# Kernel tuning notes

Hardware: AMD Instinct MI355X
Metric: run time of the kernel (lower is better)

The kernel has to match this reference:

```python
import jax, jax.numpy as jnp
import numpy as np

N = 50000
E = 800000
NEG_SLOPE = 0.2


def setup_inputs() -> dict:
    key = jax.random.key(0)
    ks = jax.random.split(key, 12)
    feat = jax.random.normal(ks[0], (N, 256), dtype=jnp.float32)
    src = jax.random.randint(ks[1], (E,), 0, N, dtype=jnp.int32)
    dst = jax.random.randint(ks[2], (E,), 0, N, dtype=jnp.int32)
    # layer 1: in=256 -> H=4, D=64 (concat 256)
    W1 = jax.random.normal(ks[3], (256, 256), dtype=jnp.float32) * (1.0 / np.sqrt(256))
    attn_l1 = jax.random.normal(ks[4], (4, 64), dtype=jnp.float32) * 0.1
    attn_r1 = jax.random.normal(ks[5], (4, 64), dtype=jnp.float32) * 0.1
    bias1 = jnp.zeros((256,), dtype=jnp.float32)
    # layer 2: in=256 -> H=1, D=128
    W2 = jax.random.normal(ks[6], (256, 128), dtype=jnp.float32) * (1.0 / np.sqrt(256))
    attn_l2 = jax.random.normal(ks[7], (1, 128), dtype=jnp.float32) * 0.1
    attn_r2 = jax.random.normal(ks[8], (1, 128), dtype=jnp.float32) * 0.1
    bias2 = jnp.zeros((128,), dtype=jnp.float32)
    return {"feat": feat, "src": src, "dst": dst,
            "W1": W1, "attn_l1": attn_l1, "attn_r1": attn_r1, "bias1": bias1,
            "W2": W2, "attn_l2": attn_l2, "attn_r2": attn_r2, "bias2": bias2}


def gat_conv(feat, src, dst, W, attn_l, attn_r, bias, apply_relu):
    H, D = attn_l.shape
    n = feat.shape[0]
    ft = (feat @ W).reshape(n, H, D)                      # [N,H,D]
    el = jnp.einsum('nhd,hd->nh', ft, attn_l)             # [N,H]
    er = jnp.einsum('nhd,hd->nh', ft, attn_r)             # [N,H]
    e = el[src] + er[dst]                                 # [E,H]  u_add_v
    e = jnp.where(e > 0, e, NEG_SLOPE * e)                # leaky_relu
    # edge softmax grouped by dst
    m = jax.ops.segment_max(e, dst, num_segments=n)       # [N,H]
    ex = jnp.exp(e - m[dst])
    denom = jax.ops.segment_sum(ex, dst, num_segments=n)  # [N,H]
    a = ex / denom[dst]                                   # [E,H]
    msg = ft[src] * a[:, :, None]                         # [E,H,D]
    out = jax.ops.segment_sum(msg, dst, num_segments=n)   # [N,H,D]
    out = out + bias.reshape(1, H, D)
    out = out.reshape(n, H * D)                           # concat_out
    if apply_relu:
        out = jax.nn.relu(out)
    return out


def reference(feat, src, dst, W1, attn_l1, attn_r1, bias1, W2, attn_l2, attn_r2, bias2):
    h = gat_conv(feat, src, dst, W1, attn_l1, attn_r1, bias1, apply_relu=True)
    h = gat_conv(h, src, dst, W2, attn_l2, attn_r2, bias2, apply_relu=False)
    return h
```

## Files before the change

kernel.cpp:

```cpp
#include <hip/hip_runtime.h>
#include <hip/hip_bf16.h>

#define NEG_SLOPE 0.2f

typedef short s16x8 __attribute__((ext_vector_type(8)));
typedef float f32x4 __attribute__((ext_vector_type(4)));

__device__ __forceinline__ unsigned short f2bf(float f) {
    unsigned int u = __float_as_uint(f);
    unsigned int r = (u + 0x7fffu + ((u >> 16) & 1u)) >> 16;
    return (unsigned short)r;
}
__device__ __forceinline__ float bf2f(unsigned int us) {
    return __uint_as_float(us << 16);
}


__global__ void count_wl_k(const int* __restrict__ dst, int* __restrict__ counts, int E,
                           const float* __restrict__ W1, const float* __restrict__ al1,
                           const float* __restrict__ ar1,
                           const float* __restrict__ W2, const float* __restrict__ al2,
                           const float* __restrict__ ar2,
                           float* __restrict__ wl1, float* __restrict__ wl2) {
    if (blockIdx.x == 0) {
        int k = threadIdx.x;
        #pragma unroll
        for (int h = 0; h < 4; h++) {
            float sl = 0.f, sr = 0.f;
            #pragma unroll 8
            for (int d = 0; d < 64; d++) {
                float wv = W1[k * 256 + h * 64 + d];
                sl = fmaf(wv, al1[h * 64 + d], sl);
                sr = fmaf(wv, ar1[h * 64 + d], sr);
            }
            wl1[k * 8 + h] = sl;
            wl1[k * 8 + 4 + h] = sr;
        }
        float sl = 0.f, sr = 0.f;
        #pragma unroll 8
        for (int d = 0; d < 128; d++) {
            float wv = W2[k * 128 + d];
            sl = fmaf(wv, al2[d], sl);
            sr = fmaf(wv, ar2[d], sr);
        }
        wl2[k * 2 + 0] = sl;
        wl2[k * 2 + 1] = sr;
        return;
    }
    int e = (blockIdx.x - 1) * 256 + threadIdx.x;
    if (e < E) atomicAdd(&counts[dst[e]], 1);
}


__global__ __launch_bounds__(1024) void scan_k(const int* __restrict__ counts,
                                               int* __restrict__ flags,
                                               int* __restrict__ offsets,
                                               int* __restrict__ cursor, int n) {
    __shared__ int s_wt[16];
    __shared__ int s_base;
    const int tid = threadIdx.x, lane = tid & 63, wid = tid >> 6;
    const int bid = blockIdx.x;
    const int i = bid * 1024 + tid;
    int v = (i < n) ? counts[i] : 0;
    int incl = v;
    #pragma unroll
    for (int o = 1; o < 64; o <<= 1) {
        int t = __shfl_up(incl, o);
        if (lane >= o) incl += t;
    }
    if (lane == 63) s_wt[wid] = incl;
    __syncthreads();
    if (tid == 0) {
        int r = 0;
        #pragma unroll
        for (int w = 0; w < 16; w++) { int t = s_wt[w]; s_wt[w] = r; r += t; }
        atomicExch(&flags[bid], r + 1);
        s_base = 0;
    }
    __syncthreads();
    if (wid == 0) {
        int contrib = 0;
        if (lane < bid) {
            int f;
            while ((f = atomicAdd(&flags[lane], 0)) == 0) {}
            contrib = f - 1;
        }
        #pragma unroll
        for (int o = 32; o > 0; o >>= 1) contrib += __shfl_xor(contrib, o);
        if (lane == 0) s_base = contrib;
    }
    __syncthreads();
    if (i < n) {
        int excl = s_base + s_wt[wid] + (incl - v);
        offsets[i + 1] = excl + v;
        cursor[i] = excl;
    }
    if (bid == 0 && tid == 0) offsets[0] = 0;
}

__global__ void fill_csr_k(const int* __restrict__ src, const int* __restrict__ dst,
                           int* __restrict__ cursor, int* __restrict__ csr_src, int E) {
    int e = blockIdx.x * blockDim.x + threadIdx.x;
    if (e < E) {
        int pos = atomicAdd(&cursor[dst[e]], 1);
        csr_src[pos] = src[e];
    }
}


template <int MODE>
__global__ __launch_bounds__(256) void gemm_k(const float* __restrict__ A,
                                              const float* __restrict__ B,
                                              unsigned short* __restrict__ Cb,
                                              int M, int K, int Nc,
                                              const float* __restrict__ wl,
                                              float* __restrict__ el,
                                              float* __restrict__ er) {
    __shared__ __align__(16) unsigned short As_hi[128][40], As_lo[128][40];
    __shared__ __align__(16) unsigned short Bs_hi[64][40],  Bs_lo[64][40];
    __shared__ float s_wla[256], s_wlb[256];
    __shared__ float s_red[128][2];

    const int tid = threadIdx.x;
    const int lane = tid & 63, wid = tid >> 6;
    const int by = blockIdx.x;
    const int row0 = blockIdx.y * 128;
    const int col0 = by * 64;
    const int wm = (wid & 1) * 64;
    const int wn = (wid >> 1) * 32;
    const int quad = lane >> 4, mrow = lane & 15;

    const int a_r = tid >> 1;
    const int a_k = (tid & 1) * 16;
    const int b_k = tid >> 3;
    const int b_n = (tid & 7) * 8;
    const bool a_valid = (row0 + a_r) < M;

    if (MODE == 1) { s_wla[tid] = wl[tid * 8 + by]; s_wlb[tid] = wl[tid * 8 + 4 + by]; }
    else           { s_wla[tid] = wl[tid * 2 + by]; }
    __syncthreads();

    f32x4 acc[4][2];
    #pragma unroll
    for (int i = 0; i < 4; i++)
        #pragma unroll
        for (int j = 0; j < 2; j++) acc[i][j] = f32x4{0.f, 0.f, 0.f, 0.f};
    float pa = 0.f, pb = 0.f;

    for (int k0 = 0; k0 < K; k0 += 32) {
        float af[16];
        if (a_valid) {
            const float* ap = &A[(size_t)(row0 + a_r) * K + k0 + a_k];
            #pragma unroll
            for (int q = 0; q < 4; q++) {
                float4 t = *(const float4*)(ap + q * 4);
                af[q * 4 + 0] = t.x; af[q * 4 + 1] = t.y;
                af[q * 4 + 2] = t.z; af[q * 4 + 3] = t.w;
            }
        } else {
            #pragma unroll
            for (int q = 0; q < 16; q++) af[q] = 0.f;
        }
        #pragma unroll
        for (int p = 0; p < 16; p++) {
            pa = fmaf(af[p], s_wla[k0 + a_k + p], pa);
            if (MODE == 1) pb = fmaf(af[p], s_wlb[k0 + a_k + p], pb);
        }
        unsigned int* dh = (unsigned int*)&As_hi[a_r][a_k];
        unsigned int* dl = (unsigned int*)&As_lo[a_r][a_k];
        #pragma unroll
        for (int p = 0; p < 8; p++) {
            unsigned short h0 = f2bf(af[2 * p]), h1 = f2bf(af[2 * p + 1]);
            unsigned short l0 = f2bf(af[2 * p] - bf2f(h0));
            unsigned short l1 = f2bf(af[2 * p + 1] - bf2f(h1));
            dh[p] = (unsigned int)h0 | ((unsigned int)h1 << 16);
            dl[p] = (unsigned int)l0 | ((unsigned int)l1 << 16);
        }
        {
            const float* bp = &B[(size_t)(k0 + b_k) * Nc + col0 + b_n];
            float4 t0 = *(const float4*)(bp);
            float4 t1 = *(const float4*)(bp + 4);
            float bf[8] = {t0.x, t0.y, t0.z, t0.w, t1.x, t1.y, t1.z, t1.w};
            #pragma unroll
            for (int x = 0; x < 8; x++) {
                unsigned short h = f2bf(bf[x]);
                unsigned short l = f2bf(bf[x] - bf2f(h));
                Bs_hi[b_n + x][b_k] = h;
                Bs_lo[b_n + x][b_k] = l;
            }
        }
        __syncthreads();

        s16x8 ah[4], al4[4], bh[2], bl[2];
        #pragma unroll
        for (int i = 0; i < 4; i++) {
            ah[i]  = *(const s16x8*)&As_hi[wm + 16 * i + mrow][quad * 8];
            al4[i] = *(const s16x8*)&As_lo[wm + 16 * i + mrow][quad * 8];
        }
        #pragma unroll
        for (int j = 0; j < 2; j++) {
            bh[j] = *(const s16x8*)&Bs_hi[wn + 16 * j + mrow][quad * 8];
            bl[j] = *(const s16x8*)&Bs_lo[wn + 16 * j + mrow][quad * 8];
        }
        #pragma unroll
        for (int i = 0; i < 4; i++)
            #pragma unroll
            for (int j = 0; j < 2; j++) {
                acc[i][j] = __builtin_amdgcn_mfma_f32_16x16x32_bf16(ah[i],  bh[j], acc[i][j], 0, 0, 0);
                acc[i][j] = __builtin_amdgcn_mfma_f32_16x16x32_bf16(ah[i],  bl[j], acc[i][j], 0, 0, 0);
                acc[i][j] = __builtin_amdgcn_mfma_f32_16x16x32_bf16(al4[i], bh[j], acc[i][j], 0, 0, 0);
            }
        __syncthreads();
    }

    if (a_k == 16) { s_red[a_r][0] = pa; if (MODE == 1) s_red[a_r][1] = pb; }
    __syncthreads();
    if (a_k == 0 && a_valid) {
        float ra = pa + s_red[a_r][0];
        if (MODE == 1) {
            float rb = pb + s_red[a_r][1];
            el[(row0 + a_r) * 4 + by] = ra;
            er[(row0 + a_r) * 4 + by] = rb;
        } else {
            (by == 0 ? el : er)[row0 + a_r] = ra;
        }
    }

    #pragma unroll
    for (int i = 0; i < 4; i++) {
        #pragma unroll
        for (int j = 0; j < 2; j++) {
            int col = col0 + wn + 16 * j + mrow;
            int rbase = row0 + wm + 16 * i + quad * 4;
            #pragma unroll
            for (int r = 0; r < 4; r++) {
                int row = rbase + r;
                if (row < M) Cb[(size_t)row * Nc + col] = f2bf(acc[i][j][r]);
            }
        }
    }
}


__device__ __forceinline__ void fma8(float* acc, float wgt, uint4 u) {
    acc[0] = fmaf(wgt, bf2f(u.x & 0xffff), acc[0]);
    acc[1] = fmaf(wgt, bf2f(u.x >> 16),    acc[1]);
    acc[2] = fmaf(wgt, bf2f(u.y & 0xffff), acc[2]);
    acc[3] = fmaf(wgt, bf2f(u.y >> 16),    acc[3]);
    acc[4] = fmaf(wgt, bf2f(u.z & 0xffff), acc[4]);
    acc[5] = fmaf(wgt, bf2f(u.z >> 16),    acc[5]);
    acc[6] = fmaf(wgt, bf2f(u.w & 0xffff), acc[6]);
    acc[7] = fmaf(wgt, bf2f(u.w >> 16),    acc[7]);
}

template <int H, int D, bool RELU>
__global__ __launch_bounds__(256) void fagg_k(const unsigned short* __restrict__ ft,
                                              const float* __restrict__ el,
                                              const float* __restrict__ er,
                                              const int* __restrict__ offsets,
                                              const int* __restrict__ csr_src,
                                              const float* __restrict__ bias,
                                              float* __restrict__ out, int n_nodes) {
    constexpr int HD = H * D;
    constexpr int LPE = HD / 8;
    constexpr int EPI = 64 / LPE;
    const int lane = threadIdx.x & 63;
    const int w = threadIdx.x >> 6;
    const int n = blockIdx.x * 4 + w;
    __shared__ int   s_src[4][64];
    __shared__ float s_a[4][64 * H];
    if (n >= n_nodes) return;
    const int off = offsets[n];
    const int deg = offsets[n + 1] - off;
    const int lane_sub = lane & (LPE - 1);
    const int q = lane / LPE;
    const int c0 = lane_sub * 8;
    const int h_of = c0 / D;

    float ern[H];
    #pragma unroll
    for (int h = 0; h < H; h++) ern[h] = er[n * H + h];

    float acc[8];
    #pragma unroll
    for (int t = 0; t < 8; t++) acc[t] = 0.f;

    const int* s_src_w = s_src[w];
    const float* s_a_w = s_a[w];
    const uint4* fp = ((const uint4*)ft) + lane_sub;

    if (deg <= 64) {
        const bool act = lane < deg;
        int sv = act ? csr_src[off + lane] : 0;
        s_src[w][lane] = sv;
        float evr[H];
        if constexpr (H == 4) {
            float4 e4 = ((const float4*)el)[sv];
            evr[0] = e4.x; evr[1] = e4.y; evr[2] = e4.z; evr[3] = e4.w;
        } else {
            evr[0] = el[sv];
        }
        int p0, p1, p2, p3;
        {
            p0 = s_src_w[q]; p1 = s_src_w[EPI + q];
            p2 = s_src_w[2 * EPI + q]; p3 = s_src_w[3 * EPI + q];
        }
        uint4 u0 = fp[(size_t)p0 * LPE];
        uint4 u1 = fp[(size_t)p1 * LPE];
        uint4 u2 = fp[(size_t)p2 * LPE];
        uint4 u3 = fp[(size_t)p3 * LPE];
        float ev[H], m[H];
        #pragma unroll
        for (int h = 0; h < H; h++) {
            float t = evr[h] + ern[h];
            t = t > 0.f ? t : NEG_SLOPE * t;
            ev[h] = act ? t : -1e30f;
            m[h] = ev[h];
        }
        #pragma unroll
        for (int h = 0; h < H; h++)
            for (int o = 32; o > 0; o >>= 1) m[h] = fmaxf(m[h], __shfl_xor(m[h], o));
        float ex[H], sm[H];
        #pragma unroll
        for (int h = 0; h < H; h++) { ex[h] = act ? __expf(ev[h] - m[h]) : 0.f; sm[h] = ex[h]; }
        #pragma unroll
        for (int h = 0; h < H; h++)
            for (int o = 32; o > 0; o >>= 1) sm[h] += __shfl_xor(sm[h], o);
        #pragma unroll
        for (int h = 0; h < H; h++)
            s_a[w][lane * H + h] = ex[h] * (sm[h] > 0.f ? 1.f / sm[h] : 0.f);
        fma8(acc, s_a_w[(q) * H + h_of], u0);
        fma8(acc, s_a_w[(EPI + q) * H + h_of], u1);
        fma8(acc, s_a_w[(2 * EPI + q) * H + h_of], u2);
        fma8(acc, s_a_w[(3 * EPI + q) * H + h_of], u3);
        const int rc = (deg + EPI - 1) & ~(EPI - 1);
        int i = 4 * EPI;
        for (; i + 4 * EPI <= rc; i += 4 * EPI) {
            int e0 = i + q, e1 = i + EPI + q, e2 = i + 2 * EPI + q, e3 = i + 3 * EPI + q;
            int s0 = s_src_w[e0], s1 = s_src_w[e1], s2 = s_src_w[e2], s3 = s_src_w[e3];
            uint4 v0 = fp[(size_t)s0 * LPE];
            uint4 v1 = fp[(size_t)s1 * LPE];
            uint4 v2 = fp[(size_t)s2 * LPE];
            uint4 v3 = fp[(size_t)s3 * LPE];
            float w0 = s_a_w[e0 * H + h_of], w1 = s_a_w[e1 * H + h_of];
            float w2 = s_a_w[e2 * H + h_of], w3 = s_a_w[e3 * H + h_of];
            fma8(acc, w0, v0); fma8(acc, w1, v1); fma8(acc, w2, v2); fma8(acc, w3, v3);
        }
        for (; i < rc; i += EPI) {
            int e = i + q;
            int s = s_src_w[e];
            uint4 v = fp[(size_t)s * LPE];
            fma8(acc, s_a_w[e * H + h_of], v);
        }
    } else {
        float m[H];
        #pragma unroll
        for (int h = 0; h < H; h++) m[h] = -1e30f;
        for (int i = lane; i < deg; i += 64) {
            int sv = csr_src[off + i];
            if constexpr (H == 4) {
                float4 e4 = ((const float4*)el)[sv];
                float tmp[4] = {e4.x, e4.y, e4.z, e4.w};
                #pragma unroll
                for (int h = 0; h < 4; h++) {
                    float t = tmp[h] + ern[h];
                    t = t > 0.f ? t : NEG_SLOPE * t;
                    m[h] = fmaxf(m[h], t);
                }
            } else {
                float t = el[sv] + ern[0];
                t = t > 0.f ? t : NEG_SLOPE * t;
                m[0] = fmaxf(m[0], t);
            }
        }
        #pragma unroll
        for (int h = 0; h < H; h++)
            for (int o = 32; o > 0; o >>= 1) m[h] = fmaxf(m[h], __shfl_xor(m[h], o));
        float sm[H];
        #pragma unroll
        for (int h = 0; h < H; h++) sm[h] = 0.f;
        for (int i = lane; i < deg; i += 64) {
            int sv = csr_src[off + i];
            if constexpr (H == 4) {
                float4 e4 = ((const float4*)el)[sv];
                float tmp[4] = {e4.x, e4.y, e4.z, e4.w};
                #pragma unroll
                for (int h = 0; h < 4; h++) {
                    float t = tmp[h] + ern[h];
                    t = t > 0.f ? t : NEG_SLOPE * t;
                    sm[h] += __expf(t - m[h]);
                }
            } else {
                float t = el[sv] + ern[0];
                t = t > 0.f ? t : NEG_SLOPE * t;
                sm[0] += __expf(t - m[0]);
            }
        }
        #pragma unroll
        for (int h = 0; h < H; h++)
            for (int o = 32; o > 0; o >>= 1) sm[h] += __shfl_xor(sm[h], o);
        float inv[H];
        #pragma unroll
        for (int h = 0; h < H; h++) inv[h] = (sm[h] > 0.f) ? (1.f / sm[h]) : 0.f;
        for (int base = 0; base < deg; base += 64) {
            const bool act2 = base + lane < deg;
            int sv = act2 ? csr_src[off + base + lane] : 0;
            s_src[w][lane] = sv;
            float exh[H];
            if constexpr (H == 4) {
                float4 e4 = ((const float4*)el)[sv];
                float tmp[4] = {e4.x, e4.y, e4.z, e4.w};
                #pragma unroll
                for (int h = 0; h < 4; h++) {
                    float t = tmp[h] + ern[h];
                    t = t > 0.f ? t : NEG_SLOPE * t;
                    exh[h] = act2 ? __expf(t - m[h]) * inv[h] : 0.f;
                }
            } else {
                float t = el[sv] + ern[0];
                t = t > 0.f ? t : NEG_SLOPE * t;
                exh[0] = act2 ? __expf(t - m[0]) * inv[0] : 0.f;
            }
            #pragma unroll
            for (int h = 0; h < H; h++) s_a[w][lane * H + h] = exh[h];
            int cnt = min(64, deg - base);
            int rc = (cnt + EPI - 1) & ~(EPI - 1);
            int i = 0;
            for (; i + 4 * EPI <= rc; i += 4 * EPI) {
                int e0 = i + q, e1 = i + EPI + q, e2 = i + 2 * EPI + q, e3 = i + 3 * EPI + q;
                int s0 = s_src_w[e0], s1 = s_src_w[e1], s2 = s_src_w[e2], s3 = s_src_w[e3];
                uint4 v0 = fp[(size_t)s0 * LPE];
                uint4 v1 = fp[(size_t)s1 * LPE];
                uint4 v2 = fp[(size_t)s2 * LPE];
                uint4 v3 = fp[(size_t)s3 * LPE];
                float w0 = s_a_w[e0 * H + h_of], w1 = s_a_w[e1 * H + h_of];
                float w2 = s_a_w[e2 * H + h_of], w3 = s_a_w[e3 * H + h_of];
                fma8(acc, w0, v0); fma8(acc, w1, v1); fma8(acc, w2, v2); fma8(acc, w3, v3);
            }
            for (; i < rc; i += EPI) {
                int e = i + q;
                int s = s_src_w[e];
                uint4 v = fp[(size_t)s * LPE];
                fma8(acc, s_a_w[e * H + h_of], v);
            }
        }
    }

    #pragma unroll
    for (int t = 0; t < 8; t++) {
        #pragma unroll
        for (int s = LPE; s < 64; s <<= 1) acc[t] += __shfl_xor(acc[t], s);
    }
    if (lane < LPE) {
        float4 b0 = ((const float4*)bias)[lane * 2];
        float4 b1 = ((const float4*)bias)[lane * 2 + 1];
        float4 o0{acc[0] + b0.x, acc[1] + b0.y, acc[2] + b0.z, acc[3] + b0.w};
        float4 o1{acc[4] + b1.x, acc[5] + b1.y, acc[6] + b1.z, acc[7] + b1.w};
        if (RELU) {
            o0.x = fmaxf(o0.x, 0.f); o0.y = fmaxf(o0.y, 0.f);
            o0.z = fmaxf(o0.z, 0.f); o0.w = fmaxf(o0.w, 0.f);
            o1.x = fmaxf(o1.x, 0.f); o1.y = fmaxf(o1.y, 0.f);
            o1.z = fmaxf(o1.z, 0.f); o1.w = fmaxf(o1.w, 0.f);
        }
        float4* op = (float4*)out + (size_t)n * (HD / 4) + lane * 2;
        op[0] = o0;
        op[1] = o1;
    }
}


extern "C" void kernel_launch(void* const* d_in, const int* in_sizes, int n_in,
                              void* d_out, int out_size, void* d_ws, size_t ws_size,
                              hipStream_t stream) {
    const float* feat    = (const float*)d_in[0];
    const int*   src     = (const int*)d_in[1];
    const int*   dst     = (const int*)d_in[2];
    const float* W1      = (const float*)d_in[3];
    const float* attn_l1 = (const float*)d_in[4];
    const float* attn_r1 = (const float*)d_in[5];
    const float* bias1   = (const float*)d_in[6];
    const float* W2      = (const float*)d_in[7];
    const float* attn_l2 = (const float*)d_in[8];
    const float* attn_r2 = (const float*)d_in[9];
    const float* bias2   = (const float*)d_in[10];
    float* out = (float*)d_out;

    const int N = in_sizes[0] / 256;
    const int E = in_sizes[1];
    const int NB = (N + 1023) / 1024;

    char* ws = (char*)d_ws;
    size_t o = 0;
    auto alloc = [&](size_t bytes) -> void* {
        void* p = ws + o;
        o = (o + bytes + 255) & ~(size_t)255;
        return p;
    };
    int* counts  = (int*)alloc((size_t)(N + 64) * 4);
    int* flags   = counts + N;
    int* cursor  = (int*)alloc((size_t)N * 4);
    int* offsets = (int*)alloc((size_t)(N + 1) * 4);
    int* csr_src = (int*)alloc((size_t)E * 4);
    float* wl1 = (float*)alloc(256 * 8 * 4);
    float* wl2 = (float*)alloc(256 * 2 * 4);
    float* el1 = (float*)alloc((size_t)N * 4 * 4);
    float* er1 = (float*)alloc((size_t)N * 4 * 4);
    float* el2 = (float*)alloc((size_t)N * 4);
    float* er2 = (float*)alloc((size_t)N * 4);
    unsigned short* ft1b = (unsigned short*)alloc((size_t)N * 256 * 2);
    float* h1 = (float*)alloc((size_t)N * 256 * 4);
    unsigned short* ft2b = ft1b;

    hipMemsetAsync(counts, 0, (size_t)(N + 64) * 4, stream);
    count_wl_k<<<1 + (E + 255) / 256, 256, 0, stream>>>(dst, counts, E,
        W1, attn_l1, attn_r1, W2, attn_l2, attn_r2, wl1, wl2);
    scan_k<<<NB, 1024, 0, stream>>>(counts, flags, offsets, cursor, N);
    fill_csr_k<<<(E + 255) / 256, 256, 0, stream>>>(src, dst, cursor, csr_src, E);

    gemm_k<1><<<dim3(4, (N + 127) / 128), 256, 0, stream>>>(feat, W1, ft1b, N, 256, 256,
                                                            wl1, el1, er1);
    fagg_k<4, 64, true><<<(N + 3) / 4, 256, 0, stream>>>(ft1b, el1, er1, offsets, csr_src,
                                                         bias1, h1, N);

    gemm_k<2><<<dim3(2, (N + 127) / 128), 256, 0, stream>>>(h1, W2, ft2b, N, 256, 128,
                                                            wl2, el2, er2);
    fagg_k<1, 128, false><<<(N + 3) / 4, 256, 0, stream>>>(ft2b, el2, er2, offsets, csr_src,
                                                           bias2, out, N);
}
```

Before: 381.5 us.

## Pre-split operands to bf16 hi/lo and fuse layer-2 prep into aggregation epilogue

```diff
diff --git a/kernel.cpp b/kernel.cpp
--- a/kernel.cpp
+++ b/kernel.cpp
@@ -1,5 +1,4 @@
 #include <hip/hip_runtime.h>
-#include <hip/hip_bf16.h>
 
 #define NEG_SLOPE 0.2f
 
@@ -21,8 +20,11 @@
                            const float* __restrict__ ar1,
                            const float* __restrict__ W2, const float* __restrict__ al2,
                            const float* __restrict__ ar2,
-                           float* __restrict__ wl1, float* __restrict__ wl2) {
-    if (blockIdx.x == 0) {
+                           float* __restrict__ wl1, float* __restrict__ wl2,
+                           unsigned short* __restrict__ Bt1h, unsigned short* __restrict__ Bt1l,
+                           unsigned short* __restrict__ Bt2h, unsigned short* __restrict__ Bt2l) {
+    const int b = blockIdx.x;
+    if (b == 0) {
         int k = threadIdx.x;
         #pragma unroll
         for (int h = 0; h < 4; h++) {
@@ -47,7 +49,35 @@
         wl2[k * 2 + 1] = sr;
         return;
     }
-    int e = (blockIdx.x - 1) * 256 + threadIdx.x;
+    if (b <= 4) {
+        int c = (b - 1) * 64 + (threadIdx.x >> 2);
+        int kq = threadIdx.x & 3;
+        #pragma unroll 8
+        for (int kk = 0; kk < 64; kk++) {
+            int k = kq + kk * 4;
+            float w = W1[k * 256 + c];
+            unsigned short h = f2bf(w);
+            unsigned short l = f2bf(w - bf2f(h));
+            Bt1h[c * 256 + k] = h;
+            Bt1l[c * 256 + k] = l;
+        }
+        return;
+    }
+    if (b <= 6) {
+        int c = (b - 5) * 64 + (threadIdx.x >> 2);
+        int kq = threadIdx.x & 3;
+        #pragma unroll 8
+        for (int kk = 0; kk < 64; kk++) {
+            int k = kq + kk * 4;
+            float w = W2[k * 128 + c];
+            unsigned short h = f2bf(w);
+            unsigned short l = f2bf(w - bf2f(h));
+            Bt2h[c * 256 + k] = h;
+            Bt2l[c * 256 + k] = l;
+        }
+        return;
+    }
+    int e = (b - 7) * 256 + threadIdx.x;
     if (e < E) atomicAdd(&counts[dst[e]], 1);
 }
 
@@ -108,99 +138,121 @@
 }
 
 
-template <int MODE>
-__global__ __launch_bounds__(256) void gemm_k(const float* __restrict__ A,
-                                              const float* __restrict__ B,
+__global__ __launch_bounds__(256) void prep_k(const float* __restrict__ feat,
+                                              const float* __restrict__ wl1,
+                                              unsigned short* __restrict__ Ah,
+                                              unsigned short* __restrict__ Al,
+                                              float* __restrict__ el1,
+                                              float* __restrict__ er1, int Nn) {
+    const int lane = threadIdx.x & 63, wid = threadIdx.x >> 6;
+    const int n = blockIdx.x * 4 + wid;
+    if (n >= Nn) return;
+    float4 f = ((const float4*)(feat + (size_t)n * 256))[lane];
+    unsigned short h0 = f2bf(f.x), h1 = f2bf(f.y), h2 = f2bf(f.z), h3 = f2bf(f.w);
+    unsigned short l0 = f2bf(f.x - bf2f(h0)), l1 = f2bf(f.y - bf2f(h1));
+    unsigned short l2 = f2bf(f.z - bf2f(h2)), l3 = f2bf(f.w - bf2f(h3));
+    uint2 hv, lv;
+    hv.x = (unsigned)h0 | ((unsigned)h1 << 16);
+    hv.y = (unsigned)h2 | ((unsigned)h3 << 16);
+    lv.x = (unsigned)l0 | ((unsigned)l1 << 16);
+    lv.y = (unsigned)l2 | ((unsigned)l3 << 16);
+    ((uint2*)(Ah + (size_t)n * 256))[lane] = hv;
+    ((uint2*)(Al + (size_t)n * 256))[lane] = lv;
+
+    float ff[4] = {f.x, f.y, f.z, f.w};
+    float pa[4] = {0.f, 0.f, 0.f, 0.f}, pb[4] = {0.f, 0.f, 0.f, 0.f};
+    const float* wp = wl1 + lane * 32;
+    #pragma unroll
+    for (int j = 0; j < 4; j++) {
+        float4 wa = *(const float4*)(wp + j * 8);
+        float4 wb = *(const float4*)(wp + j * 8 + 4);
+        pa[0] = fmaf(ff[j], wa.x, pa[0]); pa[1] = fmaf(ff[j], wa.y, pa[1]);
+        pa[2] = fmaf(ff[j], wa.z, pa[2]); pa[3] = fmaf(ff[j], wa.w, pa[3]);
+        pb[0] = fmaf(ff[j], wb.x, pb[0]); pb[1] = fmaf(ff[j], wb.y, pb[1]);
+        pb[2] = fmaf(ff[j], wb.z, pb[2]); pb[3] = fmaf(ff[j], wb.w, pb[3]);
+    }
+    #pragma unroll
+    for (int h = 0; h < 4; h++) {
+        #pragma unroll
+        for (int o = 32; o > 0; o >>= 1) {
+            pa[h] += __shfl_xor(pa[h], o);
+            pb[h] += __shfl_xor(pb[h], o);
+        }
+    }
+    if (lane == 0) {
+        ((float4*)el1)[n] = float4{pa[0], pa[1], pa[2], pa[3]};
+        ((float4*)er1)[n] = float4{pb[0], pb[1], pb[2], pb[3]};
+    }
+}
+
+
+__global__ __launch_bounds__(256) void gemm_k(const unsigned short* __restrict__ Ah,
+                                              const unsigned short* __restrict__ Al,
+                                              const unsigned short* __restrict__ Bh,
+                                              const unsigned short* __restrict__ Bl,
                                               unsigned short* __restrict__ Cb,
-                                              int M, int K, int Nc,
-                                              const float* __restrict__ wl,
-                                              float* __restrict__ el,
-                                              float* __restrict__ er) {
-    __shared__ __align__(16) unsigned short As_hi[128][40], As_lo[128][40];
-    __shared__ __align__(16) unsigned short Bs_hi[64][40],  Bs_lo[64][40];
-    __shared__ float s_wla[256], s_wlb[256];
-    __shared__ float s_red[128][2];
+                                              int M, int Nc) {
+    __shared__ __align__(16) unsigned short As_h[128][56], As_l[128][56];
+    __shared__ __align__(16) unsigned short Bs_h[64][56], Bs_l[64][56];
 
     const int tid = threadIdx.x;
     const int lane = tid & 63, wid = tid >> 6;
-    const int by = blockIdx.x;
     const int row0 = blockIdx.y * 128;
-    const int col0 = by * 64;
+    const int col0 = blockIdx.x * 64;
     const int wm = (wid & 1) * 64;
     const int wn = (wid >> 1) * 32;
     const int quad = lane >> 4, mrow = lane & 15;
 
-    const int a_r = tid >> 1;
+    const int a_row = tid >> 1;
     const int a_k = (tid & 1) * 16;
-    const int b_k = tid >> 3;
-    const int b_n = (tid & 7) * 8;
-    const bool a_valid = (row0 + a_r) < M;
-
-    if (MODE == 1) { s_wla[tid] = wl[tid * 8 + by]; s_wlb[tid] = wl[tid * 8 + 4 + by]; }
-    else           { s_wla[tid] = wl[tid * 2 + by]; }
-    __syncthreads();
+    const int b_col = tid >> 2;
+    const int b_k = (tid & 3) * 8;
+
+    const size_t a_off = (size_t)min(row0 + a_row, M - 1) * 256 + a_k;
+    const size_t b_off = (size_t)(col0 + b_col) * 256 + b_k;
 
     f32x4 acc[4][2];
     #pragma unroll
     for (int i = 0; i < 4; i++)
         #pragma unroll
         for (int j = 0; j < 2; j++) acc[i][j] = f32x4{0.f, 0.f, 0.f, 0.f};
-    float pa = 0.f, pb = 0.f;
-
-    for (int k0 = 0; k0 < K; k0 += 32) {
-        float af[16];
-        if (a_valid) {
-            const float* ap = &A[(size_t)(row0 + a_r) * K + k0 + a_k];
-            #pragma unroll
-            for (int q = 0; q < 4; q++) {
-                float4 t = *(const float4*)(ap + q * 4);
-                af[q * 4 + 0] = t.x; af[q * 4 + 1] = t.y;
-                af[q * 4 + 2] = t.z; af[q * 4 + 3] = t.w;
-            }
-        } else {
-            #pragma unroll
-            for (int q = 0; q < 16; q++) af[q] = 0.f;
-        }
-        #pragma unroll
-        for (int p = 0; p < 16; p++) {
-            pa = fmaf(af[p], s_wla[k0 + a_k + p], pa);
-            if (MODE == 1) pb = fmaf(af[p], s_wlb[k0 + a_k + p], pb);
-        }
-        unsigned int* dh = (unsigned int*)&As_hi[a_r][a_k];
-        unsigned int* dl = (unsigned int*)&As_lo[a_r][a_k];
-        #pragma unroll
-        for (int p = 0; p < 8; p++) {
-            unsigned short h0 = f2bf(af[2 * p]), h1 = f2bf(af[2 * p + 1]);
-            unsigned short l0 = f2bf(af[2 * p] - bf2f(h0));
-            unsigned short l1 = f2bf(af[2 * p + 1] - bf2f(h1));
-            dh[p] = (unsigned int)h0 | ((unsigned int)h1 << 16);
-            dl[p] = (unsigned int)l0 | ((unsigned int)l1 << 16);
-        }
-        {
-            const float* bp = &B[(size_t)(k0 + b_k) * Nc + col0 + b_n];
-            float4 t0 = *(const float4*)(bp);
-            float4 t1 = *(const float4*)(bp + 4);
-            float bf[8] = {t0.x, t0.y, t0.z, t0.w, t1.x, t1.y, t1.z, t1.w};
-            #pragma unroll
-            for (int x = 0; x < 8; x++) {
-                unsigned short h = f2bf(bf[x]);
-                unsigned short l = f2bf(bf[x] - bf2f(h));
-                Bs_hi[b_n + x][b_k] = h;
-                Bs_lo[b_n + x][b_k] = l;
-            }
-        }
+
+    uint4 rah0 = *(const uint4*)(Ah + a_off);
+    uint4 rah1 = *(const uint4*)(Ah + a_off + 8);
+    uint4 ral0 = *(const uint4*)(Al + a_off);
+    uint4 ral1 = *(const uint4*)(Al + a_off + 8);
+    uint4 rbh  = *(const uint4*)(Bh + b_off);
+    uint4 rbl  = *(const uint4*)(Bl + b_off);
+
+    for (int kt = 0; kt < 8; kt++) {
         __syncthreads();
-
+        *(uint4*)&As_h[a_row][a_k]     = rah0;
+        *(uint4*)&As_h[a_row][a_k + 8] = rah1;
+        *(uint4*)&As_l[a_row][a_k]     = ral0;
+        *(uint4*)&As_l[a_row][a_k + 8] = ral1;
+        *(uint4*)&Bs_h[b_col][b_k] = rbh;
+        *(uint4*)&Bs_l[b_col][b_k] = rbl;
+        __syncthreads();
+        if (kt < 7) {
+            size_t ao = a_off + (size_t)(kt + 1) * 32;
+            size_t bo = b_off + (size_t)(kt + 1) * 32;
+            rah0 = *(const uint4*)(Ah + ao);
+            rah1 = *(const uint4*)(Ah + ao + 8);
+            ral0 = *(const uint4*)(Al + ao);
+            ral1 = *(const uint4*)(Al + ao + 8);
+            rbh  = *(const uint4*)(Bh + bo);
+            rbl  = *(const uint4*)(Bl + bo);
+        }
         s16x8 ah[4], al4[4], bh[2], bl[2];
         #pragma unroll
         for (int i = 0; i < 4; i++) {
-            ah[i]  = *(const s16x8*)&As_hi[wm + 16 * i + mrow][quad * 8];
-            al4[i] = *(const s16x8*)&As_lo[wm + 16 * i + mrow][quad * 8];
+            ah[i]  = *(const s16x8*)&As_h[wm + 16 * i + mrow][quad * 8];
+            al4[i] = *(const s16x8*)&As_l[wm + 16 * i + mrow][quad * 8];
         }
         #pragma unroll
         for (int j = 0; j < 2; j++) {
-            bh[j] = *(const s16x8*)&Bs_hi[wn + 16 * j + mrow][quad * 8];
-            bl[j] = *(const s16x8*)&Bs_lo[wn + 16 * j + mrow][quad * 8];
+            bh[j] = *(const s16x8*)&Bs_h[wn + 16 * j + mrow][quad * 8];
+            bl[j] = *(const s16x8*)&Bs_l[wn + 16 * j + mrow][quad * 8];
         }
         #pragma unroll
         for (int i = 0; i < 4; i++)
@@ -210,20 +262,6 @@
                 acc[i][j] = __builtin_amdgcn_mfma_f32_16x16x32_bf16(ah[i],  bl[j], acc[i][j], 0, 0, 0);
                 acc[i][j] = __builtin_amdgcn_mfma_f32_16x16x32_bf16(al4[i], bh[j], acc[i][j], 0, 0, 0);
             }
-        __syncthreads();
-    }
-
-    if (a_k == 16) { s_red[a_r][0] = pa; if (MODE == 1) s_red[a_r][1] = pb; }
-    __syncthreads();
-    if (a_k == 0 && a_valid) {
-        float ra = pa + s_red[a_r][0];
-        if (MODE == 1) {
-            float rb = pb + s_red[a_r][1];
-            el[(row0 + a_r) * 4 + by] = ra;
-            er[(row0 + a_r) * 4 + by] = rb;
-        } else {
-            (by == 0 ? el : er)[row0 + a_r] = ra;
-        }
     }
 
     #pragma unroll
@@ -253,14 +291,19 @@
     acc[7] = fmaf(wgt, bf2f(u.w >> 16),    acc[7]);
 }
 
-template <int H, int D, bool RELU>
+template <int H, int D, bool RELU, bool FUSE2>
 __global__ __launch_bounds__(256) void fagg_k(const unsigned short* __restrict__ ft,
                                               const float* __restrict__ el,
                                               const float* __restrict__ er,
                                               const int* __restrict__ offsets,
                                               const int* __restrict__ csr_src,
                                               const float* __restrict__ bias,
-                                              float* __restrict__ out, int n_nodes) {
+                                              float* __restrict__ out, int n_nodes,
+                                              unsigned short* __restrict__ oh,
+                                              unsigned short* __restrict__ ol,
+                                              const float* __restrict__ wl2,
+                                              float* __restrict__ el2,
+                                              float* __restrict__ er2) {
     constexpr int HD = H * D;
     constexpr int LPE = HD / 8;
     constexpr int EPI = 64 / LPE;
@@ -454,17 +497,50 @@
     if (lane < LPE) {
         float4 b0 = ((const float4*)bias)[lane * 2];
         float4 b1 = ((const float4*)bias)[lane * 2 + 1];
-        float4 o0{acc[0] + b0.x, acc[1] + b0.y, acc[2] + b0.z, acc[3] + b0.w};
-        float4 o1{acc[4] + b1.x, acc[5] + b1.y, acc[6] + b1.z, acc[7] + b1.w};
+        float v[8] = {acc[0] + b0.x, acc[1] + b0.y, acc[2] + b0.z, acc[3] + b0.w,
+                      acc[4] + b1.x, acc[5] + b1.y, acc[6] + b1.z, acc[7] + b1.w};
         if (RELU) {
-            o0.x = fmaxf(o0.x, 0.f); o0.y = fmaxf(o0.y, 0.f);
-            o0.z = fmaxf(o0.z, 0.f); o0.w = fmaxf(o0.w, 0.f);
-            o1.x = fmaxf(o1.x, 0.f); o1.y = fmaxf(o1.y, 0.f);
-            o1.z = fmaxf(o1.z, 0.f); o1.w = fmaxf(o1.w, 0.f);
-        }
-        float4* op = (float4*)out + (size_t)n * (HD / 4) + lane * 2;
-        op[0] = o0;
-        op[1] = o1;
+            #pragma unroll
+            for (int t = 0; t < 8; t++) v[t] = fmaxf(v[t], 0.f);
+        }
+        if constexpr (FUSE2) {
+            unsigned short hh[8], ll[8];
+            #pragma unroll
+            for (int t = 0; t < 8; t++) {
+                hh[t] = f2bf(v[t]);
+                ll[t] = f2bf(v[t] - bf2f(hh[t]));
+            }
+            uint4 hv, lv;
+            hv.x = (unsigned)hh[0] | ((unsigned)hh[1] << 16);
+            hv.y = (unsigned)hh[2] | ((unsigned)hh[3] << 16);
+            hv.z = (unsigned)hh[4] | ((unsigned)hh[5] << 16);
+            hv.w = (unsigned)hh[6] | ((unsigned)hh[7] << 16);
+            lv.x = (unsigned)ll[0] | ((unsigned)ll[1] << 16);
+            lv.y = (unsigned)ll[2] | ((unsigned)ll[3] << 16);
+            lv.z = (unsigned)ll[4] | ((unsigned)ll[5] << 16);
+            lv.w = (unsigned)ll[6] | ((unsigned)ll[7] << 16);
+            ((uint4*)(oh + (size_t)n * HD))[lane] = hv;
+            ((uint4*)(ol + (size_t)n * HD))[lane] = lv;
+            float pa = 0.f, pb = 0.f;
+            #pragma unroll
+            for (int t = 0; t < 8; t++) {
+                float2 wv = ((const float2*)wl2)[lane * 8 + t];
+                pa = fmaf(v[t], wv.x, pa);
+                pb = fmaf(v[t], wv.y, pb);
+            }
+            #pragma unroll
+            for (int o = 16; o > 0; o >>= 1) {
+                pa += __shfl_xor(pa, o);
+                pb += __shfl_xor(pb, o);
+            }
+            if (lane == 0) { el2[n] = pa; er2[n] = pb; }
+        } else {
+            float4 o0{v[0], v[1], v[2], v[3]};
+            float4 o1{v[4], v[5], v[6], v[7]};
+            float4* op = (float4*)out + (size_t)n * (HD / 4) + lane * 2;
+            op[0] = o0;
+            op[1] = o1;
+        }
     }
 }
 
@@ -508,22 +584,31 @@
     float* el2 = (float*)alloc((size_t)N * 4);
     float* er2 = (float*)alloc((size_t)N * 4);
     unsigned short* ft1b = (unsigned short*)alloc((size_t)N * 256 * 2);
-    float* h1 = (float*)alloc((size_t)N * 256 * 4);
+    unsigned short* Ah   = (unsigned short*)alloc((size_t)N * 256 * 2);
+    unsigned short* Al   = (unsigned short*)alloc((size_t)N * 256 * 2);
+    unsigned short* Bt1h = (unsigned short*)alloc((size_t)256 * 256 * 2);
+    unsigned short* Bt1l = (unsigned short*)alloc((size_t)256 * 256 * 2);
+    unsigned short* Bt2h = (unsigned short*)alloc((size_t)128 * 256 * 2);
+    unsigned short* Bt2l = (unsigned short*)alloc((size_t)128 * 256 * 2);
     unsigned short* ft2b = ft1b;
+    unsigned short* h1h  = Ah;
+    unsigned short* h1l  = Al;
 
     hipMemsetAsync(counts, 0, (size_t)(N + 64) * 4, stream);
-    count_wl_k<<<1 + (E + 255) / 256, 256, 0, stream>>>(dst, counts, E,
-        W1, attn_l1, attn_r1, W2, attn_l2, attn_r2, wl1, wl2);
+    count_wl_k<<<7 + (E + 255) / 256, 256, 0, stream>>>(dst, counts, E,
+        W1, attn_l1, attn_r1, W2, attn_l2, attn_r2, wl1, wl2, Bt1h, Bt1l, Bt2h, Bt2l);
     scan_k<<<NB, 1024, 0, stream>>>(counts, flags, offsets, cursor, N);
     fill_csr_k<<<(E + 255) / 256, 256, 0, stream>>>(src, dst, cursor, csr_src, E);
-
-    gemm_k<1><<<dim3(4, (N + 127) / 128), 256, 0, stream>>>(feat, W1, ft1b, N, 256, 256,
-                                                            wl1, el1, er1);
-    fagg_k<4, 64, true><<<(N + 3) / 4, 256, 0, stream>>>(ft1b, el1, er1, offsets, csr_src,
-                                                         bias1, h1, N);
-
-    gemm_k<2><<<dim3(2, (N + 127) / 128), 256, 0, stream>>>(h1, W2, ft2b, N, 256, 128,
-                                                            wl2, el2, er2);
-    fagg_k<1, 128, false><<<(N + 3) / 4, 256, 0, stream>>>(ft2b, el2, er2, offsets, csr_src,
-                                                           bias2, out, N);
-}
+    prep_k<<<(N + 3) / 4, 256, 0, stream>>>(feat, wl1, Ah, Al, el1, er1, N);
+
+    gemm_k<<<dim3(4, (N + 127) / 128), 256, 0, stream>>>(Ah, Al, Bt1h, Bt1l, ft1b, N, 256);
+    fagg_k<4, 64, true, true><<<(N + 3) / 4, 256, 0, stream>>>(ft1b, el1, er1, offsets, csr_src,
+                                                               bias1, nullptr, N,
+                                                               h1h, h1l, wl2, el2, er2);
+
+    gemm_k<<<dim3(2, (N + 127) / 128), 256, 0, stream>>>(h1h, h1l, Bt2h, Bt2l, ft2b, N, 128);
+    fagg_k<1, 128, false, false><<<(N + 3) / 4, 256, 0, stream>>>(ft2b, el2, er2, offsets, csr_src,
+                                                                  bias2, out, N,
+                                                                  nullptr, nullptr, nullptr,
+                                                                  nullptr, nullptr);
+}
```

Result: slower. 408.8 us (+7.2%).
